# Kernel tuning notes

Measured on AMD Instinct MI355X. Metric: run time of the kernel, lower is better.

The kernel has to match this reference:

```python
import jax, jax.numpy as jnp
import numpy as np
import math

HEADS = 4
DIM_HEAD = 32
EPS = 1e-5

def _ln_channels(x):
    # LayerNorm over channel axis (axis=1) of NCHW, no affine (eps=1e-5)
    mu = jnp.mean(x, axis=1, keepdims=True)
    var = jnp.mean((x - mu) ** 2, axis=1, keepdims=True)
    return (x - mu) * jax.lax.rsqrt(var + EPS)

def setup_inputs() -> dict:
    key = jax.random.key(0)
    k1, k2, k3, k4 = jax.random.split(key, 4)
    dim, inner = 256, HEADS * DIM_HEAD
    x = jax.random.normal(k1, (16, dim, 64, 64), dtype=jnp.float32)
    Wqkv = jax.random.normal(k2, (3 * inner, dim), dtype=jnp.float32) * (1.0 / math.sqrt(dim))
    Wout = jax.random.normal(k3, (dim, inner), dtype=jnp.float32) * (1.0 / math.sqrt(inner))
    bout = jax.random.normal(k4, (dim,), dtype=jnp.float32) * 0.01
    return {"x": x, "Wqkv": Wqkv, "Wout": Wout, "bout": bout}

def reference(x, Wqkv, Wout, bout):
    B, C, H, W = x.shape
    N = H * W
    inner = HEADS * DIM_HEAD
    # pre-norm (channel-wise LayerNorm via permute in torch)
    normed = _ln_channels(x)
    # 1x1 conv to qkv: [B, 3*inner, H, W]
    qkv = jnp.einsum('oc,bchw->bohw', Wqkv, normed)
    q, k, v = jnp.split(qkv, 3, axis=1)
    # [B, inner, H, W] -> [B, heads, N, dim_head]
    def to_heads(t):
        return t.reshape(B, HEADS, DIM_HEAD, N).transpose(0, 1, 3, 2)
    q, k, v = to_heads(q), to_heads(k), to_heads(v)
    q = jax.nn.softmax(q, axis=-1)          # over dim_head
    k = jax.nn.softmax(k, axis=-2)          # over N
    q = q / math.sqrt(DIM_HEAD)
    v = v / N
    context = jnp.einsum('bhnd,bhne->bhde', k, v)   # [B,h,d,d]
    out = jnp.einsum('bhde,bhnd->bhne', context, q) # [B,h,N,d]
    out = out.transpose(0, 1, 3, 2).reshape(B, inner, H, W)
    out = jnp.einsum('oc,bchw->bohw', Wout, out) + bout[None, :, None, None]
    out = _ln_channels(out)                  # LinearAttention.out_norm
    return out + x                           # residual
```

## Files before the change

### kernel.cpp

```cpp
#include <hip/hip_runtime.h>
#include <hip/hip_bf16.h>
#include <math.h>

#define BATCH 16
#define CH 256
#define NPOS 4096
#define INNER 128
#define HEADS 4
#define DH 32

typedef __hip_bfloat16 bf16;
typedef short bf8v __attribute__((ext_vector_type(8)));
typedef float f32x4 __attribute__((ext_vector_type(4)));

__device__ __forceinline__ float b2f(bf16 v) { return __bfloat162float(v); }
__device__ __forceinline__ float us2f(unsigned short u) {
    unsigned w = ((unsigned)u) << 16; float f; __builtin_memcpy(&f, &w, 4); return f;
}
__device__ __forceinline__ unsigned short f2us(float f) {
    bf16 h = __float2bfloat16(f); unsigned short u; __builtin_memcpy(&u, &h, 2); return u;
}
__device__ __forceinline__ bf16 f2b(float v) { return __float2bfloat16(v); }

__global__ __launch_bounds__(256)
void prep_w_kernel(const float* __restrict__ Wqkv, bf16* __restrict__ wqb) {
    int idx = (blockIdx.x * 256 + threadIdx.x) * 4;
    float4 w = *(const float4*)&Wqkv[idx];
    ushort4 u;
    u.x = f2us(w.x); u.y = f2us(w.y); u.z = f2us(w.z); u.w = f2us(w.w);
    *(ushort4*)&wqb[idx] = u;
}

__global__ __launch_bounds__(256)
void fused_qkv_kernel(const float* __restrict__ x, const bf16* __restrict__ wqb,
                      bf16* __restrict__ p, float* __restrict__ ctxp) {
    __shared__ char smem[36864];
    __shared__ float stats[640];

    const int b = blockIdx.y, tile = blockIdx.x, n0 = tile * 64;
    const int tid = threadIdx.x;
    const int w = tid >> 6, lane = tid & 63;
    const int lrow = lane & 15, kq = lane >> 4;
    bf16* A = (bf16*)smem;

    {
        const int nq = tid & 15, cp = tid >> 4;
        float s[4] = {0.f,0.f,0.f,0.f}, sq[4] = {0.f,0.f,0.f,0.f};
        #pragma unroll
        for (int i = 0; i < 8; ++i) {
            int c0 = cp * 2 + 32 * i;
            const float* xp = x + ((size_t)b * CH + c0) * NPOS + n0 + nq * 4;
            float4 fa = *(const float4*)xp;
            float4 fb = *(const float4*)(xp + NPOS);
            #pragma unroll
            for (int j = 0; j < 4; ++j) {
                float va = (&fa.x)[j], vb = (&fb.x)[j];
                s[j] += va + vb; sq[j] += va * va + vb * vb;
                *(unsigned*)&A[(nq * 4 + j) * 264 + c0] =
                    (unsigned)f2us(va) | ((unsigned)f2us(vb) << 16);
            }
        }
        #pragma unroll
        for (int j = 0; j < 4; ++j) {
            s[j]  += __shfl_xor(s[j], 16, 64);  sq[j] += __shfl_xor(sq[j], 16, 64);
            s[j]  += __shfl_xor(s[j], 32, 64);  sq[j] += __shfl_xor(sq[j], 32, 64);
            if (lane < 16) {
                stats[(nq * 4 + j) * 8 + w * 2]     = s[j];
                stats[(nq * 4 + j) * 8 + w * 2 + 1] = sq[j];
            }
        }
    }
    __syncthreads();
    if (tid < 64) {
        float s  = stats[tid*8] + stats[tid*8+2] + stats[tid*8+4] + stats[tid*8+6];
        float sq = stats[tid*8+1] + stats[tid*8+3] + stats[tid*8+5] + stats[tid*8+7];
        float m = s * (1.f / 256.f);
        float var = sq * (1.f / 256.f) - m * m;
        stats[512 + tid * 2] = m;
        stats[512 + tid * 2 + 1] = rsqrtf(var + 1e-5f);
    }
    __syncthreads();
    {
        unsigned* A32 = (unsigned*)A;
        #pragma unroll 4
        for (int i = 0; i < 32; ++i) {
            int idx = i * 256 + tid;
            int c2 = idx & 127, n = idx >> 7;
            unsigned u = A32[n * 132 + c2];
            float m = stats[512 + n * 2], rs = stats[512 + n * 2 + 1];
            float v0 = (us2f((unsigned short)(u & 0xffffu)) - m) * rs;
            float v1 = (us2f((unsigned short)(u >> 16)) - m) * rs;
            A32[n * 132 + c2] = (unsigned)f2us(v0) | ((unsigned)f2us(v1) << 16);
        }
    }
    __syncthreads();

    ushort4 ekp[4][2];
    float se0 = 0.f, se1 = 0.f;

    for (int ph = 0; ph < 3; ++ph) {
        const bf16* wp = wqb + (size_t)(ph * 128 + w * 32) * 256;
        f32x4 acc[4][2];
        #pragma unroll
        for (int i = 0; i < 4; ++i) {
            acc[i][0] = (f32x4){0.f,0.f,0.f,0.f};
            acc[i][1] = (f32x4){0.f,0.f,0.f,0.f};
        }
        #pragma unroll 2
        for (int k0 = 0; k0 < 256; k0 += 32) {
            bf8v af[4], bfr[2];
            #pragma unroll
            for (int t = 0; t < 4; ++t)
                af[t] = *(const bf8v*)&A[(t * 16 + lrow) * 264 + k0 + kq * 8];
            #pragma unroll
            for (int t = 0; t < 2; ++t)
                bfr[t] = *(const bf8v*)&wp[(size_t)(t * 16 + lrow) * 256 + k0 + kq * 8];
            #pragma unroll
            for (int mt = 0; mt < 4; ++mt)
                #pragma unroll
                for (int nt = 0; nt < 2; ++nt)
                    acc[mt][nt] = __builtin_amdgcn_mfma_f32_16x16x32_bf16(
                        af[mt], bfr[nt], acc[mt][nt], 0, 0, 0);
        }

        if (ph == 0) {
            unsigned* pg32 = (unsigned*)p;
            #pragma unroll
            for (int mt = 0; mt < 4; ++mt)
                #pragma unroll
                for (int r = 0; r < 4; ++r) {
                    float e0 = __expf(b2f(f2b(acc[mt][0][r])));
                    float e1 = __expf(b2f(f2b(acc[mt][1][r])));
                    float s = e0 + e1;
                    s += __shfl_xor(s, 1, 64);  s += __shfl_xor(s, 2, 64);
                    s += __shfl_xor(s, 4, 64);  s += __shfl_xor(s, 8, 64);
                    float rd = 1.f / s;
                    int row = mt * 16 + kq * 4 + r;
                    pg32[(size_t)(b * NPOS + n0 + row) * 64 + w * 16 + lrow] =
                        (unsigned)f2us(e0 * rd) | ((unsigned)f2us(e1 * rd) << 16);
                }
        } else if (ph == 1) {
            se0 = 0.f; se1 = 0.f;
            #pragma unroll
            for (int mt = 0; mt < 4; ++mt) {
                ushort4 u0, u1;
                unsigned short q_;
                #pragma unroll
                for (int r = 0; r < 4; ++r) {
                    q_ = f2us(__expf(b2f(f2b(acc[mt][0][r]))));
                    se0 += us2f(q_); (&u0.x)[r] = q_;
                    q_ = f2us(__expf(b2f(f2b(acc[mt][1][r]))));
                    se1 += us2f(q_); (&u1.x)[r] = q_;
                }
                ekp[mt][0] = u0; ekp[mt][1] = u1;
            }
            se0 += __shfl_xor(se0, 16, 64); se0 += __shfl_xor(se0, 32, 64);
            se1 += __shfl_xor(se1, 16, 64); se1 += __shfl_xor(se1, 32, 64);
        } else {
            __syncthreads();
            bf16* ekt = (bf16*)(smem + w * 9216);
            bf16* vt  = (bf16*)(smem + w * 9216 + 4608);
            #pragma unroll
            for (int mt = 0; mt < 4; ++mt)
                #pragma unroll
                for (int nt = 0; nt < 2; ++nt) {
                    ushort4 vv;
                    vv.x = f2us(acc[mt][nt][0]); vv.y = f2us(acc[mt][nt][1]);
                    vv.z = f2us(acc[mt][nt][2]); vv.w = f2us(acc[mt][nt][3]);
                    int d = nt * 16 + lrow, n = mt * 16 + kq * 4;
                    *(ushort4*)&vt[d * 72 + n]  = vv;
                    *(ushort4*)&ekt[d * 72 + n] = ekp[mt][nt];
                }
            f32x4 cacc[2][2];
            cacc[0][0] = (f32x4){0.f,0.f,0.f,0.f}; cacc[0][1] = cacc[0][0];
            cacc[1][0] = cacc[0][0];               cacc[1][1] = cacc[0][0];
            #pragma unroll
            for (int ks = 0; ks < 2; ++ks) {
                bf8v a2[2], bv2[2];
                a2[0]  = *(const bf8v*)&ekt[lrow * 72 + ks * 32 + kq * 8];
                a2[1]  = *(const bf8v*)&ekt[(16 + lrow) * 72 + ks * 32 + kq * 8];
                bv2[0] = *(const bf8v*)&vt[lrow * 72 + ks * 32 + kq * 8];
                bv2[1] = *(const bf8v*)&vt[(16 + lrow) * 72 + ks * 32 + kq * 8];
                #pragma unroll
                for (int mt2 = 0; mt2 < 2; ++mt2)
                    #pragma unroll
                    for (int nt2 = 0; nt2 < 2; ++nt2)
                        cacc[mt2][nt2] = __builtin_amdgcn_mfma_f32_16x16x32_bf16(
                            a2[mt2], bv2[nt2], cacc[mt2][nt2], 0, 0, 0);
            }
            float* pb = ctxp + ((size_t)(b * 64 + tile) * 4 + w) * 1056;
            #pragma unroll
            for (int mt2 = 0; mt2 < 2; ++mt2)
                #pragma unroll
                for (int nt2 = 0; nt2 < 2; ++nt2)
                    #pragma unroll
                    for (int r = 0; r < 4; ++r) {
                        int d = mt2 * 16 + kq * 4 + r, e = nt2 * 16 + lrow;
                        pb[d * 32 + e] = cacc[mt2][nt2][r];
                    }
            if (kq == 0) {
                pb[1024 + lrow] = se0;
                pb[1024 + 16 + lrow] = se1;
            }
        }
    }
}

__global__ __launch_bounds__(256)
void reduce_ctx_kernel(const float* __restrict__ ctxp, float* __restrict__ ctxu,
                       float* __restrict__ separt) {
    int h = blockIdx.x, b = blockIdx.y;
    int tid = threadIdx.x;
    for (int i = 0; i < 2; ++i) {
        int idx = i * 256 + tid;
        if (idx >= 264) break;
        f32x4 s = (f32x4){0.f,0.f,0.f,0.f};
        for (int t = 0; t < 64; ++t) {
            const float* src = ctxp + ((size_t)(b * 64 + t) * 4 + h) * 1056 + idx * 4;
            s += *(const f32x4*)src;
        }
        int j = idx * 4;
        if (j < 1024) *(f32x4*)&ctxu[((size_t)(b * 4 + h)) * 1024 + j] = s;
        else          *(f32x4*)&separt[((size_t)(b * 4 + h)) * 32 + (j - 1024)] = s;
    }
}

__global__ __launch_bounds__(256)
void wmod_kernel(const float* __restrict__ Wout, const float* __restrict__ ctxu,
                 const float* __restrict__ separt, bf16* __restrict__ wmod) {
    __shared__ float cs[4096];
    __shared__ float ses[128];
    int cg = blockIdx.x, b = blockIdx.y;
    int tid = threadIdx.x;
    for (int idx = tid; idx < 4096; idx += 256) {
        int hh = idx >> 10, rest = idx & 1023;
        cs[idx] = ctxu[((size_t)(b * 4 + hh)) * 1024 + rest];
    }
    if (tid < 128) {
        int hh = tid >> 5, d = tid & 31;
        ses[tid] = separt[((size_t)(b * 4 + hh)) * 32 + d];
    }
    __syncthreads();
    int c = cg * 32 + (tid & 31);
    int g = tid >> 5;
    int h = g >> 1, d0 = (g & 1) * 16;
    const float* wr = Wout + (size_t)c * INNER + h * DH;
    float w[32];
    #pragma unroll
    for (int i = 0; i < 8; ++i) {
        float4 t = *(const float4*)&wr[i * 4];
        w[i * 4] = t.x; w[i * 4 + 1] = t.y; w[i * 4 + 2] = t.z; w[i * 4 + 3] = t.w;
    }
    const float SCALE = 4.3158341e-05f;
    #pragma unroll
    for (int dd = 0; dd < 16; ++dd) {
        int d = d0 + dd;
        const float* cr = &cs[h * 1024 + d * 32];
        float s = 0.f;
        #pragma unroll
        for (int e4 = 0; e4 < 8; ++e4) {
            f32x4 t = *(const f32x4*)&cr[e4 * 4];
            s += w[e4 * 4] * t[0] + w[e4 * 4 + 1] * t[1]
               + w[e4 * 4 + 2] * t[2] + w[e4 * 4 + 3] * t[3];
        }
        float val = s * SCALE / ses[h * 32 + d];
        wmod[((size_t)b * CH + c) * INNER + h * DH + ((d & 15) * 2 + (d >> 4))] =
            f2b(val);
    }
}

__global__ __launch_bounds__(256)
void fused_out_kernel(const bf16* __restrict__ p, const bf16* __restrict__ wmod,
                      const float* __restrict__ bout, const float* __restrict__ x,
                      float* __restrict__ out) {
    __shared__ char lds[39424];
    bf16* Ap = (bf16*)lds;
    float* ct = (float*)lds;
    float* st = (float*)(lds + 36864);

    const int b = blockIdx.y, n0 = blockIdx.x * 64;
    const int tid = threadIdx.x;
    const int w = tid >> 6, lane = tid & 63;
    const int lrow = lane & 15, kq = lane >> 4;

    {
        const uint4* pg = (const uint4*)p;
        unsigned* A32 = (unsigned*)Ap;
        #pragma unroll
        for (int i = 0; i < 4; ++i) {
            int idx = i * 256 + tid;
            int c4 = idx & 15, n = idx >> 4;
            uint4 u = pg[(size_t)(b * NPOS + n0 + n) * 16 + c4];
            *(uint4*)(A32 + n * 68 + c4 * 4) = u;
        }
    }
    __syncthreads();

    f32x4 acc[4][4];
    #pragma unroll
    for (int i = 0; i < 4; ++i)
        #pragma unroll
        for (int j = 0; j < 4; ++j) acc[i][j] = (f32x4){0.f, 0.f, 0.f, 0.f};

    const bf16* wb = wmod + (size_t)b * CH * INNER + (size_t)(w * 64) * INNER;
    #pragma unroll 2
    for (int k0 = 0; k0 < 128; k0 += 32) {
        bf8v af[4], bfr[4];
        #pragma unroll
        for (int t = 0; t < 4; ++t)
            af[t] = *(const bf8v*)&Ap[(t * 16 + lrow) * 136 + k0 + kq * 8];
        #pragma unroll
        for (int t = 0; t < 4; ++t)
            bfr[t] = *(const bf8v*)&wb[(size_t)(t * 16 + lrow) * 128 + k0 + kq * 8];
        #pragma unroll
        for (int mt = 0; mt < 4; ++mt)
            #pragma unroll
            for (int nt = 0; nt < 4; ++nt)
                acc[mt][nt] = __builtin_amdgcn_mfma_f32_16x16x32_bf16(
                    af[mt], bfr[nt], acc[mt][nt], 0, 0, 0);
    }

    #pragma unroll
    for (int nt = 0; nt < 4; ++nt) {
        float bv = bout[w * 64 + nt * 16 + lrow];
        #pragma unroll
        for (int mt = 0; mt < 4; ++mt)
            #pragma unroll
            for (int r = 0; r < 4; ++r) acc[mt][nt][r] += bv;
    }

    #pragma unroll
    for (int mt = 0; mt < 4; ++mt)
        #pragma unroll
        for (int r = 0; r < 4; ++r) {
            float s = 0.f, sq = 0.f;
            #pragma unroll
            for (int nt = 0; nt < 4; ++nt) {
                float v = acc[mt][nt][r];
                s += v; sq += v * v;
            }
            #pragma unroll
            for (int m = 1; m <= 8; m <<= 1) {
                s += __shfl_xor(s, m, 64);
                sq += __shfl_xor(sq, m, 64);
            }
            if (lrow == 0) {
                int row = mt * 16 + kq * 4 + r;
                st[w * 128 + row * 2] = s;
                st[w * 128 + row * 2 + 1] = sq;
            }
        }
    __syncthreads();
    if (tid < 64) {
        float s  = st[tid * 2]       + st[128 + tid * 2]
                 + st[256 + tid * 2] + st[384 + tid * 2];
        float sq = st[tid * 2 + 1]       + st[128 + tid * 2 + 1]
                 + st[256 + tid * 2 + 1] + st[384 + tid * 2 + 1];
        float m = s * (1.f / 256.f);
        float var = sq * (1.f / 256.f) - m * m;
        st[512 + tid * 2] = m;
        st[512 + tid * 2 + 1] = rsqrtf(var + 1e-5f);
    }
    __syncthreads();
    #pragma unroll
    for (int mt = 0; mt < 4; ++mt)
        #pragma unroll
        for (int r = 0; r < 4; ++r) {
            int row = mt * 16 + kq * 4 + r;
            float m = st[512 + row * 2], rs = st[512 + row * 2 + 1];
            #pragma unroll
            for (int nt = 0; nt < 4; ++nt)
                acc[mt][nt][r] = (acc[mt][nt][r] - m) * rs;
        }

    for (int pr = 0; pr < 2; ++pr) {
        __syncthreads();
        #pragma unroll
        for (int mi = 0; mi < 2; ++mi) {
            int mt = pr * 2 + mi;
            #pragma unroll
            for (int nt = 0; nt < 4; ++nt)
                #pragma unroll
                for (int r = 0; r < 4; ++r) {
                    int rl = mi * 16 + kq * 4 + r;
                    ct[(w * 64 + nt * 16 + lrow) * 36 + rl] = acc[mt][nt][r];
                }
        }
        __syncthreads();
        #pragma unroll
        for (int i = 0; i < 8; ++i) {
            int idx = i * 256 + tid;
            int n4 = (idx & 7) * 4, c = idx >> 3;
            size_t gi = ((size_t)b * CH + c) * NPOS + n0 + pr * 32 + n4;
            f32x4 cv = *(const f32x4*)&ct[c * 36 + n4];
            float4 xv = *(const float4*)&x[gi];
            float4 ov;
            ov.x = cv[0] + xv.x; ov.y = cv[1] + xv.y;
            ov.z = cv[2] + xv.z; ov.w = cv[3] + xv.w;
            *(float4*)&out[gi] = ov;
        }
    }
}

extern "C" void kernel_launch(void* const* d_in, const int* in_sizes, int n_in,
                              void* d_out, int out_size, void* d_ws, size_t ws_size,
                              hipStream_t stream) {
    const float* x    = (const float*)d_in[0];
    const float* Wqkv = (const float*)d_in[1];
    const float* Wout = (const float*)d_in[2];
    const float* bout = (const float*)d_in[3];
    float* out = (float*)d_out;

    char* ws = (char*)d_ws;
    bf16*  p      = (bf16*)ws;
    float* ctxp   = (float*)(ws + 16777216);
    float* ctxu   = (float*)(ws + 34078720);
    float* separt = (float*)(ws + 34340864);
    bf16*  wmod   = (bf16*)(ws + 34349056);
    bf16*  wqb    = (bf16*)(ws + 35397632);

    prep_w_kernel<<<dim3(96), 256, 0, stream>>>(Wqkv, wqb);
    fused_qkv_kernel<<<dim3(64, BATCH), 256, 0, stream>>>(x, wqb, p, ctxp);
    reduce_ctx_kernel<<<dim3(4, BATCH), 256, 0, stream>>>(ctxp, ctxu, separt);
    wmod_kernel<<<dim3(8, BATCH), 256, 0, stream>>>(Wout, ctxu, separt, wmod);
    fused_out_kernel<<<dim3(64, BATCH), 256, 0, stream>>>(p, wmod, bout, x, out);
}
```

Measured before the change: 194.0 us.

## Fold LayerNorm into GEMM epilogue, merge ctx reduction with wmod, prefetch residual

Drops the in-shared-memory LayerNorm pass over the bf16 activation tile. Instead the GEMM runs on raw x and the normalisation is applied afterwards as (acc - mu*rowsum(W))*rstd, using weight row sums computed in prep_w_kernel. It also merges the context reduction and Wout modulation kernels into one launch, and prefetches residual x into registers before the output LayerNorm. The aim is to remove a smem pass, two syncs and a kernel launch, at the risk of worse precision from running the bf16 GEMM on unnormalised inputs.

Measured after the change: 209.9 us. 1.08x slower.

```diff
diff --git a/kernel.cpp b/kernel.cpp
--- a/kernel.cpp
+++ b/kernel.cpp
@@ -23,16 +23,23 @@
 __device__ __forceinline__ bf16 f2b(float v) { return __float2bfloat16(v); }
 
 __global__ __launch_bounds__(256)
-void prep_w_kernel(const float* __restrict__ Wqkv, bf16* __restrict__ wqb) {
+void prep_w_kernel(const float* __restrict__ Wqkv, bf16* __restrict__ wqb,
+                   float* __restrict__ wqs) {
     int idx = (blockIdx.x * 256 + threadIdx.x) * 4;
     float4 w = *(const float4*)&Wqkv[idx];
     ushort4 u;
     u.x = f2us(w.x); u.y = f2us(w.y); u.z = f2us(w.z); u.w = f2us(w.w);
     *(ushort4*)&wqb[idx] = u;
+    float s4 = us2f(u.x) + us2f(u.y) + us2f(u.z) + us2f(u.w);
+    #pragma unroll
+    for (int m = 1; m <= 32; m <<= 1) s4 += __shfl_xor(s4, m, 64);
+    if ((threadIdx.x & 63) == 0)
+        wqs[blockIdx.x * 4 + (threadIdx.x >> 6)] = s4;
 }
 
 __global__ __launch_bounds__(256)
 void fused_qkv_kernel(const float* __restrict__ x, const bf16* __restrict__ wqb,
+                      const float* __restrict__ wqs,
                       bf16* __restrict__ p, float* __restrict__ ctxp) {
     __shared__ char smem[36864];
     __shared__ float stats[640];
@@ -80,26 +87,14 @@
         stats[512 + tid * 2 + 1] = rsqrtf(var + 1e-5f);
     }
     __syncthreads();
-    {
-        unsigned* A32 = (unsigned*)A;
-        #pragma unroll 4
-        for (int i = 0; i < 32; ++i) {
-            int idx = i * 256 + tid;
-            int c2 = idx & 127, n = idx >> 7;
-            unsigned u = A32[n * 132 + c2];
-            float m = stats[512 + n * 2], rs = stats[512 + n * 2 + 1];
-            float v0 = (us2f((unsigned short)(u & 0xffffu)) - m) * rs;
-            float v1 = (us2f((unsigned short)(u >> 16)) - m) * rs;
-            A32[n * 132 + c2] = (unsigned)f2us(v0) | ((unsigned)f2us(v1) << 16);
-        }
-    }
-    __syncthreads();
 
     ushort4 ekp[4][2];
     float se0 = 0.f, se1 = 0.f;
 
     for (int ph = 0; ph < 3; ++ph) {
         const bf16* wp = wqb + (size_t)(ph * 128 + w * 32) * 256;
+        const float cs0 = wqs[ph * 128 + w * 32 + lrow];
+        const float cs1 = wqs[ph * 128 + w * 32 + 16 + lrow];
         f32x4 acc[4][2];
         #pragma unroll
         for (int i = 0; i < 4; ++i) {
@@ -129,13 +124,14 @@
             for (int mt = 0; mt < 4; ++mt)
                 #pragma unroll
                 for (int r = 0; r < 4; ++r) {
-                    float e0 = __expf(b2f(f2b(acc[mt][0][r])));
-                    float e1 = __expf(b2f(f2b(acc[mt][1][r])));
+                    int row = mt * 16 + kq * 4 + r;
+                    float mu = stats[512 + row * 2], rsn = stats[512 + row * 2 + 1];
+                    float e0 = __expf(b2f(f2b((acc[mt][0][r] - mu * cs0) * rsn)));
+                    float e1 = __expf(b2f(f2b((acc[mt][1][r] - mu * cs1) * rsn)));
                     float s = e0 + e1;
                     s += __shfl_xor(s, 1, 64);  s += __shfl_xor(s, 2, 64);
                     s += __shfl_xor(s, 4, 64);  s += __shfl_xor(s, 8, 64);
                     float rd = 1.f / s;
-                    int row = mt * 16 + kq * 4 + r;
                     pg32[(size_t)(b * NPOS + n0 + row) * 64 + w * 16 + lrow] =
                         (unsigned)f2us(e0 * rd) | ((unsigned)f2us(e1 * rd) << 16);
                 }
@@ -147,9 +143,11 @@
                 unsigned short q_;
                 #pragma unroll
                 for (int r = 0; r < 4; ++r) {
-                    q_ = f2us(__expf(b2f(f2b(acc[mt][0][r]))));
+                    int row = mt * 16 + kq * 4 + r;
+                    float mu = stats[512 + row * 2], rsn = stats[512 + row * 2 + 1];
+                    q_ = f2us(__expf(b2f(f2b((acc[mt][0][r] - mu * cs0) * rsn))));
                     se0 += us2f(q_); (&u0.x)[r] = q_;
-                    q_ = f2us(__expf(b2f(f2b(acc[mt][1][r]))));
+                    q_ = f2us(__expf(b2f(f2b((acc[mt][1][r] - mu * cs1) * rsn))));
                     se1 += us2f(q_); (&u1.x)[r] = q_;
                 }
                 ekp[mt][0] = u0; ekp[mt][1] = u1;
@@ -164,9 +162,14 @@
             for (int mt = 0; mt < 4; ++mt)
                 #pragma unroll
                 for (int nt = 0; nt < 2; ++nt) {
+                    float csx = nt ? cs1 : cs0;
                     ushort4 vv;
-                    vv.x = f2us(acc[mt][nt][0]); vv.y = f2us(acc[mt][nt][1]);
-                    vv.z = f2us(acc[mt][nt][2]); vv.w = f2us(acc[mt][nt][3]);
+                    #pragma unroll
+                    for (int r = 0; r < 4; ++r) {
+                        int row = mt * 16 + kq * 4 + r;
+                        float mu = stats[512 + row * 2], rsn = stats[512 + row * 2 + 1];
+                        (&vv.x)[r] = f2us((acc[mt][nt][r] - mu * csx) * rsn);
+                    }
                     int d = nt * 16 + lrow, n = mt * 16 + kq * 4;
                     *(ushort4*)&vt[d * 72 + n]  = vv;
                     *(ushort4*)&ekt[d * 72 + n] = ekp[mt][nt];
@@ -207,65 +210,55 @@
 }
 
 __global__ __launch_bounds__(256)
-void reduce_ctx_kernel(const float* __restrict__ ctxp, float* __restrict__ ctxu,
-                       float* __restrict__ separt) {
-    int h = blockIdx.x, b = blockIdx.y;
+void ctx_wmod_kernel(const float* __restrict__ ctxp, const float* __restrict__ Wout,
+                     bf16* __restrict__ wmod) {
+    __shared__ float cs[1056];
+    int h = blockIdx.x, b = blockIdx.y, ch = blockIdx.z;
     int tid = threadIdx.x;
+
+    #pragma unroll
     for (int i = 0; i < 2; ++i) {
-        int idx = i * 256 + tid;
-        if (idx >= 264) break;
-        f32x4 s = (f32x4){0.f,0.f,0.f,0.f};
-        for (int t = 0; t < 64; ++t) {
-            const float* src = ctxp + ((size_t)(b * 64 + t) * 4 + h) * 1056 + idx * 4;
-            s += *(const f32x4*)src;
-        }
-        int j = idx * 4;
-        if (j < 1024) *(f32x4*)&ctxu[((size_t)(b * 4 + h)) * 1024 + j] = s;
-        else          *(f32x4*)&separt[((size_t)(b * 4 + h)) * 32 + (j - 1024)] = s;
-    }
-}
-
-__global__ __launch_bounds__(256)
-void wmod_kernel(const float* __restrict__ Wout, const float* __restrict__ ctxu,
-                 const float* __restrict__ separt, bf16* __restrict__ wmod) {
-    __shared__ float cs[4096];
-    __shared__ float ses[128];
-    int cg = blockIdx.x, b = blockIdx.y;
-    int tid = threadIdx.x;
-    for (int idx = tid; idx < 4096; idx += 256) {
-        int hh = idx >> 10, rest = idx & 1023;
-        cs[idx] = ctxu[((size_t)(b * 4 + hh)) * 1024 + rest];
-    }
-    if (tid < 128) {
-        int hh = tid >> 5, d = tid & 31;
-        ses[tid] = separt[((size_t)(b * 4 + hh)) * 32 + d];
-    }
-    __syncthreads();
-    int c = cg * 32 + (tid & 31);
-    int g = tid >> 5;
-    int h = g >> 1, d0 = (g & 1) * 16;
+        int s = i * 256 + tid;
+        if (s < 264) {
+            f32x4 a = (f32x4){0.f,0.f,0.f,0.f};
+            const float* src = ctxp + (size_t)(b * 64 * 4 + h) * 1056 + s * 4;
+            for (int t = 0; t < 64; ++t)
+                a += *(const f32x4*)(src + (size_t)t * 4 * 1056);
+            *(f32x4*)&cs[s * 4] = a;
+        }
+    }
+    __syncthreads();
+
+    int c = ch * 128 + (tid >> 1);
+    int dh = tid & 1;
     const float* wr = Wout + (size_t)c * INNER + h * DH;
-    float w[32];
+    float wv[32];
     #pragma unroll
     for (int i = 0; i < 8; ++i) {
         float4 t = *(const float4*)&wr[i * 4];
-        w[i * 4] = t.x; w[i * 4 + 1] = t.y; w[i * 4 + 2] = t.z; w[i * 4 + 3] = t.w;
+        wv[i * 4] = t.x; wv[i * 4 + 1] = t.y; wv[i * 4 + 2] = t.z; wv[i * 4 + 3] = t.w;
     }
     const float SCALE = 4.3158341e-05f;
-    #pragma unroll
-    for (int dd = 0; dd < 16; ++dd) {
-        int d = d0 + dd;
-        const float* cr = &cs[h * 1024 + d * 32];
-        float s = 0.f;
+    unsigned* wm32 = (unsigned*)(wmod + ((size_t)b * CH + c) * INNER + h * DH);
+    #pragma unroll
+    for (int dd = 0; dd < 8; ++dd) {
+        int d1 = dh * 8 + dd, d2 = d1 + 16;
+        const float* c1 = &cs[d1 * 32];
+        const float* c2 = &cs[d2 * 32];
+        float s1 = 0.f, s2 = 0.f;
         #pragma unroll
         for (int e4 = 0; e4 < 8; ++e4) {
-            f32x4 t = *(const f32x4*)&cr[e4 * 4];
-            s += w[e4 * 4] * t[0] + w[e4 * 4 + 1] * t[1]
-               + w[e4 * 4 + 2] * t[2] + w[e4 * 4 + 3] * t[3];
-        }
-        float val = s * SCALE / ses[h * 32 + d];
-        wmod[((size_t)b * CH + c) * INNER + h * DH + ((d & 15) * 2 + (d >> 4))] =
-            f2b(val);
+            f32x4 t1 = *(const f32x4*)&c1[e4 * 4];
+            f32x4 t2 = *(const f32x4*)&c2[e4 * 4];
+            #pragma unroll
+            for (int j = 0; j < 4; ++j) {
+                s1 += wv[e4 * 4 + j] * t1[j];
+                s2 += wv[e4 * 4 + j] * t2[j];
+            }
+        }
+        float v1 = s1 * SCALE / cs[1024 + d1];
+        float v2 = s2 * SCALE / cs[1024 + d2];
+        wm32[d1] = (unsigned)f2us(v1) | ((unsigned)f2us(v2) << 16);
     }
 }
 
@@ -327,6 +320,14 @@
         for (int mt = 0; mt < 4; ++mt)
             #pragma unroll
             for (int r = 0; r < 4; ++r) acc[mt][nt][r] += bv;
+    }
+
+    float4 xr[4];
+    #pragma unroll
+    for (int i = 0; i < 4; ++i) {
+        int idx = i * 256 + tid;
+        int n4 = (idx & 7) * 4, c = idx >> 3;
+        xr[i] = *(const float4*)&x[((size_t)b * CH + c) * NPOS + n0 + n4];
     }
 
     #pragma unroll
@@ -373,6 +374,7 @@
                 acc[mt][nt][r] = (acc[mt][nt][r] - m) * rs;
         }
 
+    #pragma unroll 1
     for (int pr = 0; pr < 2; ++pr) {
         __syncthreads();
         #pragma unroll
@@ -388,7 +390,19 @@
         }
         __syncthreads();
         #pragma unroll
-        for (int i = 0; i < 8; ++i) {
+        for (int i = 0; i < 4; ++i) {
+            int idx = i * 256 + tid;
+            int n4 = (idx & 7) * 4, c = idx >> 3;
+            size_t gi = ((size_t)b * CH + c) * NPOS + n0 + pr * 32 + n4;
+            f32x4 cv = *(const f32x4*)&ct[c * 36 + n4];
+            float4 xv = xr[i];
+            float4 ov;
+            ov.x = cv[0] + xv.x; ov.y = cv[1] + xv.y;
+            ov.z = cv[2] + xv.z; ov.w = cv[3] + xv.w;
+            *(float4*)&out[gi] = ov;
+        }
+        #pragma unroll
+        for (int i = 4; i < 8; ++i) {
             int idx = i * 256 + tid;
             int n4 = (idx & 7) * 4, c = idx >> 3;
             size_t gi = ((size_t)b * CH + c) * NPOS + n0 + pr * 32 + n4;
@@ -399,6 +413,14 @@
             ov.z = cv[2] + xv.z; ov.w = cv[3] + xv.w;
             *(float4*)&out[gi] = ov;
         }
+        if (pr == 0) {
+            #pragma unroll
+            for (int i = 0; i < 4; ++i) {
+                int idx = i * 256 + tid;
+                int n4 = (idx & 7) * 4, c = idx >> 3;
+                xr[i] = *(const float4*)&x[((size_t)b * CH + c) * NPOS + n0 + 32 + n4];
+            }
+        }
     }
 }
 
@@ -414,14 +436,12 @@
     char* ws = (char*)d_ws;
     bf16*  p      = (bf16*)ws;
     float* ctxp   = (float*)(ws + 16777216);
-    float* ctxu   = (float*)(ws + 34078720);
-    float* separt = (float*)(ws + 34340864);
     bf16*  wmod   = (bf16*)(ws + 34349056);
     bf16*  wqb    = (bf16*)(ws + 35397632);
-
-    prep_w_kernel<<<dim3(96), 256, 0, stream>>>(Wqkv, wqb);
-    fused_qkv_kernel<<<dim3(64, BATCH), 256, 0, stream>>>(x, wqb, p, ctxp);
-    reduce_ctx_kernel<<<dim3(4, BATCH), 256, 0, stream>>>(ctxp, ctxu, separt);
-    wmod_kernel<<<dim3(8, BATCH), 256, 0, stream>>>(Wout, ctxu, separt, wmod);
+    float* wqs    = (float*)(ws + 35594240);
+
+    prep_w_kernel<<<dim3(96), 256, 0, stream>>>(Wqkv, wqb, wqs);
+    fused_qkv_kernel<<<dim3(64, BATCH), 256, 0, stream>>>(x, wqb, wqs, p, ctxp);
+    ctx_wmod_kernel<<<dim3(HEADS, BATCH, 2), 256, 0, stream>>>(ctxp, Wout, wmod);
     fused_out_kernel<<<dim3(64, BATCH), 256, 0, stream>>>(p, wmod, bout, x, out);
 }
```
